# Kernel optimization log

Measured on AMD Instinct MI355X. Metric: run time of the kernel, lower is better.

The kernel has to match this reference:

```python
import jax, jax.numpy as jnp
import numpy as np
from jax import lax

SCALE = 128.0        # x/y/w/h scale = model input size
MIN_SCORE = 0.5      # min_score_thresh
IOU_THRESH = 0.3     # mediapipe min_suppression_threshold
MAX_DET = 64         # fixed detection slots (jit-safe replacement for dynamic list)
NUM_ANCHORS = 896


def _decode(raw_boxes, anchors):
    # raw_boxes [B,A,16], anchors [A,4] = (x_center, y_center, w, h)
    ax, ay, aw, ah = anchors[:, 0], anchors[:, 1], anchors[:, 2], anchors[:, 3]
    xc = raw_boxes[..., 0] / SCALE * aw + ax
    yc = raw_boxes[..., 1] / SCALE * ah + ay
    w = raw_boxes[..., 2] / SCALE * aw
    h = raw_boxes[..., 3] / SCALE * ah
    box = jnp.stack([yc - h / 2, xc - w / 2, yc + h / 2, xc + w / 2], axis=-1)  # [B,A,4] ymin,xmin,ymax,xmax
    kp = raw_boxes[..., 4:16].reshape(*raw_boxes.shape[:-1], 6, 2)  # [B,A,6,2] (x,y)
    kpx = kp[..., 0] / SCALE * aw[:, None] + ax[:, None]
    kpy = kp[..., 1] / SCALE * ah[:, None] + ay[:, None]
    kps = jnp.stack([kpx, kpy], axis=-1).reshape(*raw_boxes.shape[:-1], 12)
    return jnp.concatenate([box, kps], axis=-1)  # [B,A,16]


def _iou(box, boxes):
    # box [4], boxes [A,4]; coords = ymin,xmin,ymax,xmax
    ymin = jnp.maximum(box[0], boxes[:, 0])
    xmin = jnp.maximum(box[1], boxes[:, 1])
    ymax = jnp.minimum(box[2], boxes[:, 2])
    xmax = jnp.minimum(box[3], boxes[:, 3])
    inter = jnp.maximum(ymax - ymin, 0.0) * jnp.maximum(xmax - xmin, 0.0)
    a1 = jnp.maximum(box[2] - box[0], 0.0) * jnp.maximum(box[3] - box[1], 0.0)
    a2 = jnp.maximum(boxes[:, 2] - boxes[:, 0], 0.0) * jnp.maximum(boxes[:, 3] - boxes[:, 1], 0.0)
    return inter / jnp.maximum(a1 + a2 - inter, 1e-6)


def _weighted_nms_single(coords, scores):
    # coords [A,16], scores [A] -> out [MAX_DET,17] sorted by descending score, zero-padded
    rem = jnp.where(scores >= MIN_SCORE, scores, -1.0)

    def step(rem, _):
        idx = jnp.argmax(rem)
        best = rem[idx]
        iou = _iou(coords[idx, :4], coords[:, :4])
        overlap = (iou > IOU_THRESH) & (rem > 0.0)
        wts = jnp.where(overlap, scores, 0.0)            # weight = candidate score
        denom = jnp.maximum(wts.sum(), 1e-6)
        blended = (coords * wts[:, None]).sum(0) / denom  # weighted box + keypoints
        det = jnp.concatenate([blended, best[None]])
        det = jnp.where(best > 0.0, det, jnp.zeros(17, det.dtype))
        rem = jnp.where(overlap, -1.0, rem)
        return rem, det

    _, out = lax.scan(step, rem, None, length=MAX_DET)
    return out


def _project(dets, matrix):
    # dets [B,MAX_DET,17], matrix [B,8] (first two rows of row-major 4x4 affine)
    m = matrix[:, None, :]  # [B,1,8]
    x_idx = jnp.array([1, 3, 4, 6, 8, 10, 12, 14])
    y_idx = jnp.array([0, 2, 5, 7, 9, 11, 13, 15])
    xs = dets[..., x_idx]
    ys = dets[..., y_idx]
    new_x = xs * m[..., 0:1] + ys * m[..., 1:2] + m[..., 3:4]
    new_y = xs * m[..., 4:5] + ys * m[..., 5:6] + m[..., 7:8]
    out = dets.at[..., x_idx].set(new_x)
    out = out.at[..., y_idx].set(new_y)
    # keep padded (invalid) rows zero, like the segmented-tensor original
    valid = dets[..., 16:17] > 0.0
    return jnp.where(valid, out, 0.0)


def _rescale(dets, h, w):
    hf = jnp.float32(h)
    wf = jnp.float32(w)
    scale = jnp.concatenate([
        jnp.array([1.0, 1.0]) * 0 + jnp.stack([hf, wf]),   # ymin*h, xmin*w
        jnp.stack([hf, wf]),                               # ymax*h, xmax*w
        jnp.tile(jnp.stack([wf, hf]), 6),                  # kp x*w, kp y*h
        jnp.ones((1,), jnp.float32),                       # score unchanged
    ])
    return dets * scale


def setup_inputs() -> dict:
    key = jax.random.key(0)
    k1, k2, k3, k4 = jax.random.split(key, 4)
    B = 2048
    return {
        "raw_boxes": jax.random.normal(k1, (B, NUM_ANCHORS, 16), jnp.float32),
        "raw_scores": jax.random.normal(k2, (B, NUM_ANCHORS), jnp.float32),
        "anchors": jax.random.uniform(k3, (NUM_ANCHORS, 4), jnp.float32),
        "transform_matrix": jax.random.normal(k4, (B, 8), jnp.float32),
        "h": 720,
        "w": 1280,
    }


def reference(raw_boxes, raw_scores, anchors, transform_matrix, h, w):
    coords = _decode(raw_boxes, anchors)                       # [B,A,16]
    scores = jax.nn.sigmoid(jnp.clip(raw_scores, -100.0, 100.0))
    dets = jax.vmap(_weighted_nms_single)(coords, scores)      # [B,MAX_DET,17]
    dets = _project(dets, transform_matrix)
    dets = _rescale(dets, h, w)
    return dets
```

## Files before the change

### kernel.cpp

```cpp
#include <hip/hip_runtime.h>
#include <math.h>

#define NANCH 896
#define MAXD 64
#define NS 14

__device__ __forceinline__ float selv17(const float d[17], int c) {
    float v = d[0];
#pragma unroll
    for (int k = 1; k < 17; ++k) v = (c == k) ? d[k] : v;
    return v;
}

__global__ __launch_bounds__(256, 2) void blaze_wave_kernel(
    const float* __restrict__ raw_boxes,
    const float* __restrict__ raw_scores,
    const float* __restrict__ anchors,
    const float* __restrict__ tmat,
    const int* __restrict__ hptr,
    const int* __restrict__ wptr,
    float* __restrict__ out,
    int B)
{
    __shared__ float sdet[4][17];
    const int lane = threadIdx.x & 63;
    const int wv   = threadIdx.x >> 6;
    const int b    = blockIdx.x * 4 + wv;
    if (b >= B) return;

    const float* rb = raw_boxes  + (size_t)b * (NANCH * 16);
    const float* rs = raw_scores + (size_t)b * NANCH;
    const float inv = 1.f / 128.f;

    const float* M = tmat + (size_t)b * 8;
    const float m0 = M[0], m1 = M[1], m3 = M[3];
    const float m4 = M[4], m5 = M[5], m7 = M[7];
    const float hf = (float)(*hptr);
    const float wf = (float)(*wptr);

    float xv[NS];
#pragma unroll
    for (int j = 0; j < NS; ++j) xv[j] = rs[lane + 64 * j];

    bool  act[NS];
    float4 r0v[NS], anv[NS];
#pragma unroll
    for (int j = 0; j < NS; ++j) {
        act[j] = (xv[j] >= 0.f);
        const int a2 = act[j] ? (lane + 64 * j) : 0;
        r0v[j] = *(const float4*)(rb + a2 * 16);
        anv[j] = *(const float4*)(anchors + a2 * 4);
    }

    float rem[NS];
#pragma unroll
    for (int j = 0; j < NS; ++j) {
        float x = fminf(fmaxf(xv[j], -100.f), 100.f);
        float s = 1.f / (1.f + expf(-x));
        rem[j] = act[j] ? s : -1.f;
    }

    float b0[NS], b1[NS], b2[NS], b3[NS], ar[NS];
#pragma unroll
    for (int j = 0; j < NS; ++j) {
        float xc = r0v[j].x * inv * anv[j].z + anv[j].x;
        float yc = r0v[j].y * inv * anv[j].w + anv[j].y;
        float ww = r0v[j].z * inv * anv[j].z;
        float hh = r0v[j].w * inv * anv[j].w;
        b0[j] = yc - hh * 0.5f; b1[j] = xc - ww * 0.5f;
        b2[j] = yc + hh * 0.5f; b3[j] = xc + ww * 0.5f;
        ar[j] = fmaxf(b2[j] - b0[j], 0.f) * fmaxf(b3[j] - b1[j], 0.f);
    }

    float* ob = out + (size_t)b * (MAXD * 17);

    int iter = 0;
    while (true) {
        float bv = -2.f; int bi = 1 << 30;
#pragma unroll
        for (int j = 0; j < NS; ++j) {
            if (rem[j] > bv) { bv = rem[j]; bi = lane + 64 * j; }
        }
#pragma unroll
        for (int s2 = 32; s2 >= 1; s2 >>= 1) {
            float ov = __shfl_xor(bv, s2, 64);
            int   oi = __shfl_xor(bi, s2, 64);
            if (ov > bv || (ov == bv && oi < bi)) { bv = ov; bi = oi; }
        }

        if (bv <= 0.f) {
            int n = (MAXD - iter) * 17;
            float* op = ob + iter * 17;
            for (int e = lane; e < n; e += 64) op[e] = 0.f;
            break;
        }

        const int bl = bi & 63, bj = bi >> 6;
        float vb0 = b0[0], vb1 = b1[0], vb2 = b2[0], vb3 = b3[0];
#pragma unroll
        for (int j = 1; j < NS; ++j) {
            if (bj == j) { vb0 = b0[j]; vb1 = b1[j]; vb2 = b2[j]; vb3 = b3[j]; }
        }
        const float bby0 = __shfl(vb0, bl, 64);
        const float bbx0 = __shfl(vb1, bl, 64);
        const float bby1 = __shfl(vb2, bl, 64);
        const float bbx1 = __shfl(vb3, bl, 64);
        const float a1 = fmaxf(bby1 - bby0, 0.f) * fmaxf(bbx1 - bbx0, 0.f);

        float acc[16];
#pragma unroll
        for (int c = 0; c < 16; ++c) acc[c] = 0.f;
        float wsum = 0.f;
        bool anyov = false;

#pragma unroll
        for (int j = 0; j < NS; ++j) {
            if (rem[j] > 0.f) {
                float yA = fmaxf(bby0, b0[j]);
                float xA = fmaxf(bbx0, b1[j]);
                float yB = fminf(bby1, b2[j]);
                float xB = fminf(bbx1, b3[j]);
                float inter = fmaxf(yB - yA, 0.f) * fmaxf(xB - xA, 0.f);
                float iou = inter / fmaxf(a1 + ar[j] - inter, 1e-6f);
                if (iou > 0.3f) {
                    anyov = true;
                    float wj = rem[j];
                    rem[j] = -1.f;
                    wsum += wj;
                    acc[0] += b0[j] * wj; acc[1] += b1[j] * wj;
                    acc[2] += b2[j] * wj; acc[3] += b3[j] * wj;
                    const int a = lane + 64 * j;
                    float4 an = *(const float4*)(anchors + a * 4);
                    const float* rp = rb + a * 16;
                    float4 r1 = *(const float4*)(rp + 4);
                    float4 r2 = *(const float4*)(rp + 8);
                    float4 r3 = *(const float4*)(rp + 12);
                    acc[4]  += (r1.x * inv * an.z + an.x) * wj;
                    acc[5]  += (r1.y * inv * an.w + an.y) * wj;
                    acc[6]  += (r1.z * inv * an.z + an.x) * wj;
                    acc[7]  += (r1.w * inv * an.w + an.y) * wj;
                    acc[8]  += (r2.x * inv * an.z + an.x) * wj;
                    acc[9]  += (r2.y * inv * an.w + an.y) * wj;
                    acc[10] += (r2.z * inv * an.z + an.x) * wj;
                    acc[11] += (r2.w * inv * an.w + an.y) * wj;
                    acc[12] += (r3.x * inv * an.z + an.x) * wj;
                    acc[13] += (r3.y * inv * an.w + an.y) * wj;
                    acc[14] += (r3.z * inv * an.z + an.x) * wj;
                    acc[15] += (r3.w * inv * an.w + an.y) * wj;
                }
            }
        }

        bool stuck = (__ballot(anyov) == 0ull);

        float det[17];
        if (!stuck) {
#pragma unroll
            for (int s2 = 32; s2 >= 1; s2 >>= 1) {
                wsum += __shfl_xor(wsum, s2, 64);
#pragma unroll
                for (int c = 0; c < 16; ++c) acc[c] += __shfl_xor(acc[c], s2, 64);
            }
            float dnm = fmaxf(wsum, 1e-6f);
#pragma unroll
            for (int c = 0; c < 16; ++c) det[c] = acc[c] / dnm;
        } else {
#pragma unroll
            for (int c = 0; c < 16; ++c) det[c] = 0.f;
        }
        det[16] = bv;

        {
            const int xi[8] = { 1, 3, 4, 6, 8, 10, 12, 14 };
            const int yi[8] = { 0, 2, 5, 7, 9, 11, 13, 15 };
#pragma unroll
            for (int k = 0; k < 8; ++k) {
                float x = det[xi[k]], y = det[yi[k]];
                det[xi[k]] = (x * m0 + y * m1 + m3) * wf;
                det[yi[k]] = (x * m4 + y * m5 + m7) * hf;
            }
        }

        if (stuck) {
            if (lane < 17) sdet[wv][lane] = selv17(det, lane);
            int n = (MAXD - iter) * 17;
            float* op = ob + iter * 17;
            int c = lane % 17;
            for (int e = lane; e < n; e += 64) {
                op[e] = sdet[wv][c];
                c += 13; if (c >= 17) c -= 17;
            }
            break;
        } else {
            if (lane < 17) ob[iter * 17 + lane] = selv17(det, lane);
            ++iter;
            if (iter == MAXD) break;
        }
    }
}

extern "C" void kernel_launch(void* const* d_in, const int* in_sizes, int n_in,
                              void* d_out, int out_size, void* d_ws, size_t ws_size,
                              hipStream_t stream) {
    (void)n_in; (void)out_size; (void)d_ws; (void)ws_size;
    const float* raw_boxes  = (const float*)d_in[0];
    const float* raw_scores = (const float*)d_in[1];
    const float* anchors    = (const float*)d_in[2];
    const float* tmat       = (const float*)d_in[3];
    const int*   hptr       = (const int*)d_in[4];
    const int*   wptr       = (const int*)d_in[5];
    float* out = (float*)d_out;

    const int B = in_sizes[0] / (NANCH * 16);
    blaze_wave_kernel<<<(B + 3) / 4, 256, 0, stream>>>(raw_boxes, raw_scores, anchors,
                                                       tmat, hptr, wptr, out, B);
}
```

Before: 198.4 us.

## Cache boxes in LDS, fast-path single-lane reductions, lane-parallel projection

Each wave stores its decoded boxes in shared memory, so the winning box is read with one LDS load instead of a 14-way select plus four shuffles. The IoU test is reordered to compute the intersection first and check rem afterwards. When only one lane holds overlapping candidates, the 6-step butterfly reduction of 17 values is replaced by direct broadcasts from that lane. The projection step is now spread across lanes using a pair shuffle instead of being done redundantly in every lane. This adds 57KB of LDS per block, which may limit occupancy.

```diff
diff --git a/kernel.cpp b/kernel.cpp
--- a/kernel.cpp
+++ b/kernel.cpp
@@ -4,13 +4,6 @@
 #define NANCH 896
 #define MAXD 64
 #define NS 14
-
-__device__ __forceinline__ float selv17(const float d[17], int c) {
-    float v = d[0];
-#pragma unroll
-    for (int k = 1; k < 17; ++k) v = (c == k) ? d[k] : v;
-    return v;
-}
 
 __global__ __launch_bounds__(256, 2) void blaze_wave_kernel(
     const float* __restrict__ raw_boxes,
@@ -22,7 +15,9 @@
     float* __restrict__ out,
     int B)
 {
-    __shared__ float sdet[4][17];
+    __shared__ float4 sbox[4][NANCH];
+    __shared__ float  sdet[4][17];
+
     const int lane = threadIdx.x & 63;
     const int wv   = threadIdx.x >> 6;
     const int b    = blockIdx.x * 4 + wv;
@@ -70,9 +65,11 @@
         b0[j] = yc - hh * 0.5f; b1[j] = xc - ww * 0.5f;
         b2[j] = yc + hh * 0.5f; b3[j] = xc + ww * 0.5f;
         ar[j] = fmaxf(b2[j] - b0[j], 0.f) * fmaxf(b3[j] - b1[j], 0.f);
+        sbox[wv][lane + 64 * j] = make_float4(b0[j], b1[j], b2[j], b3[j]);
     }
 
     float* ob = out + (size_t)b * (MAXD * 17);
+    const bool isx = (lane < 16) && ((0x555Au >> lane) & 1u);
 
     int iter = 0;
     while (true) {
@@ -95,16 +92,8 @@
             break;
         }
 
-        const int bl = bi & 63, bj = bi >> 6;
-        float vb0 = b0[0], vb1 = b1[0], vb2 = b2[0], vb3 = b3[0];
-#pragma unroll
-        for (int j = 1; j < NS; ++j) {
-            if (bj == j) { vb0 = b0[j]; vb1 = b1[j]; vb2 = b2[j]; vb3 = b3[j]; }
-        }
-        const float bby0 = __shfl(vb0, bl, 64);
-        const float bbx0 = __shfl(vb1, bl, 64);
-        const float bby1 = __shfl(vb2, bl, 64);
-        const float bbx1 = __shfl(vb3, bl, 64);
+        float4 bb = sbox[wv][bi];
+        const float bby0 = bb.x, bbx0 = bb.y, bby1 = bb.z, bbx1 = bb.w;
         const float a1 = fmaxf(bby1 - bby0, 0.f) * fmaxf(bbx1 - bbx0, 0.f);
 
         float acc[16];
@@ -115,14 +104,14 @@
 
 #pragma unroll
         for (int j = 0; j < NS; ++j) {
-            if (rem[j] > 0.f) {
-                float yA = fmaxf(bby0, b0[j]);
-                float xA = fmaxf(bbx0, b1[j]);
-                float yB = fminf(bby1, b2[j]);
-                float xB = fminf(bbx1, b3[j]);
-                float inter = fmaxf(yB - yA, 0.f) * fmaxf(xB - xA, 0.f);
+            float yA = fmaxf(bby0, b0[j]);
+            float xA = fmaxf(bbx0, b1[j]);
+            float yB = fminf(bby1, b2[j]);
+            float xB = fminf(bbx1, b3[j]);
+            float inter = fmaxf(yB - yA, 0.f) * fmaxf(xB - xA, 0.f);
+            if (inter > 0.f) {
                 float iou = inter / fmaxf(a1 + ar[j] - inter, 1e-6f);
-                if (iou > 0.3f) {
+                if (iou > 0.3f && rem[j] > 0.f) {
                     anyov = true;
                     float wj = rem[j];
                     rem[j] = -1.f;
@@ -151,38 +140,44 @@
             }
         }
 
-        bool stuck = (__ballot(anyov) == 0ull);
-
-        float det[17];
-        if (!stuck) {
+        const unsigned long long mm = __ballot(anyov);
+        const bool stuck = (mm == 0ull);
+
+        float tot[16]; float ws;
+        if (stuck) {
+#pragma unroll
+            for (int c = 0; c < 16; ++c) tot[c] = 0.f;
+            ws = 0.f;
+        } else if (__popcll(mm) == 1) {
+            const int src = (int)__ffsll((long long)mm) - 1;
+#pragma unroll
+            for (int c = 0; c < 16; ++c) tot[c] = __shfl(acc[c], src, 64);
+            ws = __shfl(wsum, src, 64);
+        } else {
 #pragma unroll
             for (int s2 = 32; s2 >= 1; s2 >>= 1) {
                 wsum += __shfl_xor(wsum, s2, 64);
 #pragma unroll
                 for (int c = 0; c < 16; ++c) acc[c] += __shfl_xor(acc[c], s2, 64);
             }
-            float dnm = fmaxf(wsum, 1e-6f);
-#pragma unroll
-            for (int c = 0; c < 16; ++c) det[c] = acc[c] / dnm;
-        } else {
-#pragma unroll
-            for (int c = 0; c < 16; ++c) det[c] = 0.f;
-        }
-        det[16] = bv;
-
-        {
-            const int xi[8] = { 1, 3, 4, 6, 8, 10, 12, 14 };
-            const int yi[8] = { 0, 2, 5, 7, 9, 11, 13, 15 };
-#pragma unroll
-            for (int k = 0; k < 8; ++k) {
-                float x = det[xi[k]], y = det[yi[k]];
-                det[xi[k]] = (x * m0 + y * m1 + m3) * wf;
-                det[yi[k]] = (x * m4 + y * m5 + m7) * hf;
-            }
-        }
+#pragma unroll
+            for (int c = 0; c < 16; ++c) tot[c] = acc[c];
+            ws = wsum;
+        }
+
+        float q = tot[0];
+#pragma unroll
+        for (int k = 1; k < 16; ++k) q = (lane == k) ? tot[k] : q;
+        const float dnm = fmaxf(ws, 1e-6f);
+        q = q / dnm;
+        const float p = __shfl(q, lane ^ 1, 64);
+        float detc;
+        if (lane >= 16) detc = bv;
+        else detc = isx ? (q * m0 + p * m1 + m3) * wf
+                        : (p * m4 + q * m5 + m7) * hf;
 
         if (stuck) {
-            if (lane < 17) sdet[wv][lane] = selv17(det, lane);
+            if (lane < 17) sdet[wv][lane] = detc;
             int n = (MAXD - iter) * 17;
             float* op = ob + iter * 17;
             int c = lane % 17;
@@ -192,7 +187,7 @@
             }
             break;
         } else {
-            if (lane < 17) ob[iter * 17 + lane] = selv17(det, lane);
+            if (lane < 17) ob[iter * 17 + lane] = detc;
             ++iter;
             if (iter == MAXD) break;
         }
```

After: 184.5 us. -7.0%, faster.
